# Optimization experiments

Measured on AMD Instinct MI355X. Metric: run time of the kernel, lower is better.

The kernel has to match this reference:

```python
import jax, jax.numpy as jnp
import numpy as np

N = 512      # state dim n
K = 8        # num_regimes
H = 256      # hidden dim for g0/g1/gate MLPs
B = 8192     # batch
INIT_SCALE = 0.1


def _mlp(x, w1, b1, w2, b2, w3, b3):
    # 2 hidden SiLU layers + linear head (matches ScalarMLP/GateNet with num_layers=2)
    h = jax.nn.silu(x @ w1 + b1)
    h = jax.nn.silu(h @ w2 + b2)
    return h @ w3 + b3


def setup_inputs() -> dict:
    key = jax.random.key(0)
    ks = jax.random.split(key, 12)

    def lin(k, fi, fo):
        kw, kb = jax.random.split(k)
        s = 1.0 / np.sqrt(fi)  # torch nn.Linear default init range
        w = jax.random.uniform(kw, (fi, fo), minval=-s, maxval=s, dtype=jnp.float32)
        b = jax.random.uniform(kb, (fo,), minval=-s, maxval=s, dtype=jnp.float32)
        return w, b

    g0_w1, g0_b1 = lin(ks[0], N, H)
    g0_w2, g0_b2 = lin(ks[1], H, H)
    g0_w3, g0_b3 = lin(ks[2], H, 1)
    g1_w1, g1_b1 = lin(ks[3], N, H)
    g1_w2, g1_b2 = lin(ks[4], H, H)
    g1_w3, g1_b3 = lin(ks[5], H, 1)
    gt_w1, gt_b1 = lin(ks[6], N, H)
    gt_w2, gt_b2 = lin(ks[7], H, H)
    gt_w3, gt_b3 = lin(ks[8], H, K)
    W = jax.random.uniform(ks[9], (K, N, N), minval=-INIT_SCALE, maxval=INIT_SCALE, dtype=jnp.float32)
    z = jax.random.normal(ks[10], (B, 2 * N), dtype=jnp.float32)
    return dict(z=z,
                g0_w1=g0_w1, g0_b1=g0_b1, g0_w2=g0_w2, g0_b2=g0_b2, g0_w3=g0_w3, g0_b3=g0_b3,
                g1_w1=g1_w1, g1_b1=g1_b1, g1_w2=g1_w2, g1_b2=g1_b2, g1_w3=g1_w3, g1_b3=g1_b3,
                gt_w1=gt_w1, gt_b1=gt_b1, gt_w2=gt_w2, gt_b2=gt_b2, gt_w3=gt_w3, gt_b3=gt_b3,
                W=W)


def reference(z,
              g0_w1, g0_b1, g0_w2, g0_b2, g0_w3, g0_b3,
              g1_w1, g1_b1, g1_w2, g1_b2, g1_w3, g1_b3,
              gt_w1, gt_b1, gt_w2, gt_b2, gt_w3, gt_b3,
              W):
    n = W.shape[-1]
    x0, x1 = z[:, :n], z[:, n:]

    def U(x0_, x1_):
        e0 = jnp.sum(_mlp(x0_, g0_w1, g0_b1, g0_w2, g0_b2, g0_w3, g0_b3))  # scalar
        e1 = jnp.sum(_mlp(x1_, g1_w1, g1_b1, g1_w2, g1_b2, g1_w3, g1_b3))
        alpha = jax.nn.softmax(_mlp(x0_, gt_w1, gt_b1, gt_w2, gt_b2, gt_w3, gt_b3), axis=-1)  # [B,K]
        # per-sample per-regime bilinear x1^T W_k x0 -> avoids materializing [B,n,n] W_eff
        q = jnp.einsum('bi,kij,bj->bk', x1_, W, x0_)
        return e0 + e1 + jnp.sum(alpha * q)

    grad_x0, grad_x1 = jax.grad(U, argnums=(0, 1))(x0, x1)
    return jnp.concatenate([-grad_x0, -grad_x1], axis=-1)  # [B, 2n]
```

## Files before the change

kernel.cpp:

```cpp
#include <hip/hip_runtime.h>
#include <cstdint>
#include <cstddef>

constexpr int BTOT = 8192, N = 512, H = 256, K = 8;

typedef __attribute__((ext_vector_type(8))) short short8v;
typedef __attribute__((ext_vector_type(4))) float f32x4;

__device__ __forceinline__ float bf2f(unsigned short u) {
    return __uint_as_float(((uint32_t)u) << 16);
}
__device__ __forceinline__ unsigned short f2bf(float f) {
    uint32_t u = __float_as_uint(f);
    uint32_t r = (u + 0x7FFFu + ((u >> 16) & 1u)) >> 16;
    return (unsigned short)r;
}

typedef __attribute__((address_space(3))) unsigned int lds_uint;
typedef __attribute__((address_space(1))) const unsigned int glob_uint;
__device__ __forceinline__ void async16(const unsigned short* g, unsigned short* l) {
    __builtin_amdgcn_global_load_lds((glob_uint*)g, (lds_uint*)l, 16, 0, 0);
}

struct GArg {
    const unsigned short* A;
    const unsigned short* Bt;
    const float* bias;
    const unsigned short* dmul;
    const float* alpha;
    const unsigned short* vsub;
    unsigned short* ob;
    unsigned short* ob2;
    float* of;
    int lda, ldbt, Ka, lddm, ldob, ldof;
};

enum { EPI_BF = 0, EPI_FWD = 1, EPI_BWD2 = 2, EPI_NEG = 3, EPI_NEGV = 4 };

template<int EPI>
__global__ __launch_bounds__(256) void gemm_g(GArg ga0, GArg ga1, GArg ga2)
{
    const int z = blockIdx.z;
    const GArg g = (z == 0) ? ga0 : (z == 1) ? ga1 : ga2;

    __shared__ __attribute__((aligned(16))) unsigned short As[3][128 * 32];
    __shared__ __attribute__((aligned(16))) unsigned short Bs[3][128 * 32];
    const int tid = threadIdx.x;
    const int lane = tid & 63, wave = tid >> 6;
    const int m0 = blockIdx.y * 128, n0 = blockIdx.x * 128;
    const int wr = (wave >> 1) * 64, wc = (wave & 1) * 64;
    const int rr = lane & 15;
    const int kb = ((lane >> 4) ^ (lane & 3)) << 3;

    const int r0 = tid >> 2;
    const int ko0 = (((tid & 3) ^ (r0 & 3)) << 3);
    const unsigned short* gA0 = g.A + (size_t)(m0 + r0) * g.lda + ko0;
    const unsigned short* gA1 = g.A + (size_t)(m0 + r0 + 64) * g.lda + ko0;
    const unsigned short* gB0 = g.Bt + (size_t)(n0 + r0) * g.ldbt + ko0;
    const unsigned short* gB1 = g.Bt + (size_t)(n0 + r0 + 64) * g.ldbt + ko0;

    auto stage = [&](int t, int buf) {
        const int k0 = t << 5;
        async16(gA0 + k0, &As[buf][tid * 8]);
        async16(gA1 + k0, &As[buf][(tid + 256) * 8]);
        async16(gB0 + k0, &Bs[buf][tid * 8]);
        async16(gB1 + k0, &Bs[buf][(tid + 256) * 8]);
    };

    f32x4 acc[4][4];
    #pragma unroll
    for (int i = 0; i < 4; ++i)
        #pragma unroll
        for (int j = 0; j < 4; ++j) acc[i][j] = (f32x4){0.f, 0.f, 0.f, 0.f};

    const int nt = g.Ka >> 5;

    stage(0, 0);
    if (nt > 1) stage(1, 1);

    int buf = 0;
    for (int t = 0; t < nt; ++t) {
        if (t + 1 < nt) { asm volatile("s_waitcnt vmcnt(4)" ::: "memory"); }
        else            { asm volatile("s_waitcnt vmcnt(0)" ::: "memory"); }
        __builtin_amdgcn_s_barrier();
        if (t + 2 < nt) {
            int b2 = buf + 2; if (b2 >= 3) b2 -= 3;
            stage(t + 2, b2);
        }
        short8v af[4], bfr[4];
        #pragma unroll
        for (int i = 0; i < 4; ++i)
            af[i] = *(const short8v*)(&As[buf][(wr + i * 16 + rr) * 32 + kb]);
        #pragma unroll
        for (int j = 0; j < 4; ++j)
            bfr[j] = *(const short8v*)(&Bs[buf][(wc + j * 16 + rr) * 32 + kb]);
        #pragma unroll
        for (int i = 0; i < 4; ++i)
            #pragma unroll
            for (int j = 0; j < 4; ++j)
                acc[i][j] = __builtin_amdgcn_mfma_f32_16x16x32_bf16(af[i], bfr[j], acc[i][j], 0, 0, 0);
        if (++buf == 3) buf = 0;
    }

    const int orow = (lane >> 4) * 4;
    #pragma unroll
    for (int i = 0; i < 4; ++i) {
        #pragma unroll
        for (int e = 0; e < 4; ++e) {
            const int row = m0 + wr + i * 16 + orow + e;
            if constexpr (EPI == EPI_NEGV) {
                float al[K];
                #pragma unroll
                for (int kk = 0; kk < K; ++kk) al[kk] = g.alpha[(size_t)row * K + kk];
                #pragma unroll
                for (int j = 0; j < 4; ++j) {
                    const int col = n0 + wc + rr + j * 16;
                    const unsigned short* vp = g.vsub + (size_t)row * (K * N) + col;
                    float sub = 0.f;
                    #pragma unroll
                    for (int kk = 0; kk < K; ++kk) sub += al[kk] * bf2f(vp[(size_t)kk * N]);
                    g.of[(size_t)row * g.ldof + col] = -acc[i][j][e] - sub;
                }
            } else {
                #pragma unroll
                for (int j = 0; j < 4; ++j) {
                    const int col = n0 + wc + rr + j * 16;
                    float v = acc[i][j][e];
                    if constexpr (EPI == EPI_BF) {
                        g.ob[(size_t)row * g.ldob + col] = f2bf(v);
                    } else if constexpr (EPI == EPI_FWD) {
                        float p = v + g.bias[col];
                        float s = 1.f / (1.f + expf(-p));
                        if (g.ob) g.ob[(size_t)row * g.ldob + col] = f2bf(p * s);
                        g.ob2[(size_t)row * g.ldob + col] = f2bf(s * (1.f + p * (1.f - s)));
                    } else if constexpr (EPI == EPI_BWD2) {
                        float t = v * bf2f(g.dmul[(size_t)row * g.lddm + col]);
                        g.ob[(size_t)row * g.ldob + col] = f2bf(t);
                    } else if constexpr (EPI == EPI_NEG) {
                        g.of[(size_t)row * g.ldof + col] -= v;
                    }
                }
            }
        }
    }
}

__global__ __launch_bounds__(256) void k_cvt_z(const float* __restrict__ z,
                                               unsigned short* __restrict__ o) {
    int g = (blockIdx.x * 256 + threadIdx.x) * 4;
    float4 v = *(const float4*)(z + g);
    ushort4 u;
    u.x = f2bf(v.x); u.y = f2bf(v.y); u.z = f2bf(v.z); u.w = f2bf(v.w);
    *(ushort4*)(o + g) = u;
}

__global__ __launch_bounds__(256) void k_transpose_w(const float* __restrict__ W,
    unsigned short* __restrict__ Wbf, unsigned short* __restrict__ WTbf)
{
    __shared__ float t[32][33];
    int k = blockIdx.z;
    int i0 = blockIdx.y * 32, j0 = blockIdx.x * 32;
    int tj = threadIdx.x & 31, ti = threadIdx.x >> 5;
    const float* Wk = W + (size_t)k * N * N;
    #pragma unroll
    for (int r = 0; r < 32; r += 8) {
        float v = Wk[(size_t)(i0 + ti + r) * N + j0 + tj];
        t[ti + r][tj] = v;
        Wbf[(size_t)k * N * N + (size_t)(i0 + ti + r) * N + j0 + tj] = f2bf(v);
    }
    __syncthreads();
    #pragma unroll
    for (int r = 0; r < 32; r += 8)
        WTbf[(size_t)k * N * N + (size_t)(j0 + ti + r) * N + i0 + tj] = f2bf(t[tj][ti + r]);
}

struct CvtJob { const float* src; unsigned short* dst; int ls, ld, cols32, tiles, trans; };
struct CvtTable { CvtJob j[12]; };

__global__ __launch_bounds__(256) void k_cvt_w(CvtTable T)
{
    int t = blockIdx.x;
    int ji = 0;
    while (t >= T.j[ji].tiles) { t -= T.j[ji].tiles; ++ji; }
    CvtJob jb = T.j[ji];
    int i0 = (t / jb.cols32) * 32, c0 = (t % jb.cols32) * 32;
    int tc = threadIdx.x & 31, tr = threadIdx.x >> 5;
    if (!jb.trans) {
        #pragma unroll
        for (int r = 0; r < 32; r += 8)
            jb.dst[(size_t)(i0 + tr + r) * jb.ld + c0 + tc] =
                f2bf(jb.src[(size_t)(i0 + tr + r) * jb.ls + c0 + tc]);
    } else {
        __shared__ float tt[32][33];
        #pragma unroll
        for (int r = 0; r < 32; r += 8)
            tt[tr + r][tc] = jb.src[(size_t)(i0 + tr + r) * jb.ls + c0 + tc];
        __syncthreads();
        #pragma unroll
        for (int r = 0; r < 32; r += 8)
            jb.dst[(size_t)(c0 + tr + r) * jb.ld + i0 + tc] = f2bf(tt[tc][tr + r]);
    }
}

__global__ __launch_bounds__(256) void k_head_s(const unsigned short* __restrict__ h2t,
    const float* __restrict__ w3t, const float* __restrict__ b3t,
    float* __restrict__ s)
{
    int t = threadIdx.x;
    int bl = t >> 3, k = t & 7;
    int b = blockIdx.x * 32 + bl;
    const unsigned short* ar = h2t + (size_t)b * H;
    float acc = b3t[k];
    for (int h0 = 0; h0 < H; h0 += 8) {
        short8v hv = *(const short8v*)(ar + h0);
        #pragma unroll
        for (int u = 0; u < 8; ++u)
            acc += bf2f((unsigned short)hv[u]) * w3t[(h0 + u) * K + k];
    }
    s[b * K + k] = acc;
}

__global__ __launch_bounds__(256) void k_q(const unsigned short* __restrict__ v0,
    const unsigned short* __restrict__ zb, float* __restrict__ q)
{
    int w = threadIdx.x >> 6, lane = threadIdx.x & 63;
    int idx = blockIdx.x * 4 + w;
    int b = idx >> 3, k = idx & 7;
    const unsigned short* vr = v0 + ((size_t)b * K + k) * N;
    const unsigned short* xr = zb + (size_t)b * 1024 + 512;
    short8v vv = *(const short8v*)(vr + lane * 8);
    short8v xv = *(const short8v*)(xr + lane * 8);
    float s = 0.f;
    #pragma unroll
    for (int t = 0; t < 8; ++t)
        s += bf2f((unsigned short)vv[t]) * bf2f((unsigned short)xv[t]);
    for (int off = 32; off; off >>= 1) s += __shfl_down(s, off, 64);
    if (lane == 0) q[idx] = s;
}

__global__ __launch_bounds__(256) void k_d(const float* __restrict__ s,
    const float* __restrict__ q, float* __restrict__ alpha,
    float* __restrict__ dd, int Bc)
{
    int b = blockIdx.x * 256 + threadIdx.x;
    if (b >= Bc) return;
    float sv[K], qv[K];
    float m = -1e30f;
    #pragma unroll
    for (int k = 0; k < K; ++k) { sv[k] = s[b * K + k]; m = fmaxf(m, sv[k]); }
    float sum = 0.f;
    #pragma unroll
    for (int k = 0; k < K; ++k) { sv[k] = expf(sv[k] - m); sum += sv[k]; }
    float inv = 1.f / sum, qbar = 0.f;
    #pragma unroll
    for (int k = 0; k < K; ++k) { sv[k] *= inv; qv[k] = q[b * K + k]; qbar += sv[k] * qv[k]; }
    #pragma unroll
    for (int k = 0; k < K; ++k) {
        alpha[b * K + k] = sv[k];
        dd[b * K + k] = sv[k] * (qv[k] - qbar);
    }
}

__global__ __launch_bounds__(256) void k_u2(
    const unsigned short* __restrict__ d2_0, const unsigned short* __restrict__ d2_1,
    const unsigned short* __restrict__ d2_t,
    const float* __restrict__ w3_0, const float* __restrict__ w3_1,
    const float* __restrict__ w3t, const float* __restrict__ dd,
    unsigned short* __restrict__ u2_0, unsigned short* __restrict__ u2_1,
    unsigned short* __restrict__ u2_t)
{
    int g = blockIdx.x * 256 + threadIdx.x;
    int h = g & (H - 1), b = g >> 8;
    u2_0[g] = f2bf(w3_0[h] * bf2f(d2_0[g]));
    u2_1[g] = f2bf(w3_1[h] * bf2f(d2_1[g]));
    float s = 0.f;
    #pragma unroll
    for (int k = 0; k < K; ++k) s += w3t[h * K + k] * dd[b * K + k];
    u2_t[g] = f2bf(s * bf2f(d2_t[g]));
}

__global__ __launch_bounds__(256) void k_gxq2(const unsigned short* __restrict__ v0,
    const unsigned short* __restrict__ v1, const float* __restrict__ alpha,
    float* __restrict__ out)
{
    int g = blockIdx.x * 256 + threadIdx.x;
    int b = g >> 6, jb = (g & 63) << 3;
    float al[K];
    #pragma unroll
    for (int k = 0; k < K; ++k) al[k] = alpha[b * K + k];
    const unsigned short* pv0 = v0 + (size_t)b * K * N + jb;
    const unsigned short* pv1 = v1 + (size_t)b * K * N + jb;
    float s0[8] = {}, s1[8] = {};
    #pragma unroll
    for (int k = 0; k < K; ++k) {
        short8v w1 = *(const short8v*)(pv1 + (size_t)k * N);
        short8v w0 = *(const short8v*)(pv0 + (size_t)k * N);
        #pragma unroll
        for (int t = 0; t < 8; ++t) {
            s0[t] += al[k] * bf2f((unsigned short)w1[t]);
            s1[t] += al[k] * bf2f((unsigned short)w0[t]);
        }
    }
    float* o0 = out + (size_t)b * 1024 + jb;
    float* o1 = o0 + 512;
    float4 x0 = *(float4*)o0, x1 = *(float4*)(o0 + 4);
    x0.x -= s0[0]; x0.y -= s0[1]; x0.z -= s0[2]; x0.w -= s0[3];
    x1.x -= s0[4]; x1.y -= s0[5]; x1.z -= s0[6]; x1.w -= s0[7];
    *(float4*)o0 = x0; *(float4*)(o0 + 4) = x1;
    float4 y0 = *(float4*)o1, y1 = *(float4*)(o1 + 4);
    y0.x -= s1[0]; y0.y -= s1[1]; y0.z -= s1[2]; y0.w -= s1[3];
    y1.x -= s1[4]; y1.y -= s1[5]; y1.z -= s1[6]; y1.w -= s1[7];
    *(float4*)o1 = y0; *(float4*)(o1 + 4) = y1;
}

extern "C" void kernel_launch(void* const* d_in, const int* in_sizes, int n_in,
                              void* d_out, int out_size, void* d_ws, size_t ws_size,
                              hipStream_t stream) {
    const float* z     = (const float*)d_in[0];
    const float* g0_w1 = (const float*)d_in[1];  const float* g0_b1 = (const float*)d_in[2];
    const float* g0_w2 = (const float*)d_in[3];  const float* g0_b2 = (const float*)d_in[4];
    const float* g0_w3 = (const float*)d_in[5];
    const float* g1_w1 = (const float*)d_in[7];  const float* g1_b1 = (const float*)d_in[8];
    const float* g1_w2 = (const float*)d_in[9];  const float* g1_b2 = (const float*)d_in[10];
    const float* g1_w3 = (const float*)d_in[11];
    const float* gt_w1 = (const float*)d_in[13]; const float* gt_b1 = (const float*)d_in[14];
    const float* gt_w2 = (const float*)d_in[15]; const float* gt_b2 = (const float*)d_in[16];
    const float* gt_w3 = (const float*)d_in[17]; const float* gt_b3 = (const float*)d_in[18];
    const float* W     = (const float*)d_in[19];
    float* out = (float*)d_out;

    char* wsb = (char*)d_ws;
    size_t off = 0;
    auto aus = [&](size_t n) -> unsigned short* {
        unsigned short* r = (unsigned short*)(wsb + off);
        off += ((n * 2 + 255) & ~(size_t)255);
        return r;
    };
    auto af4 = [&](size_t n) -> float* {
        float* r = (float*)(wsb + off);
        off += ((n * 4 + 255) & ~(size_t)255);
        return r;
    };

    unsigned short* Zbf  = aus((size_t)BTOT * 1024);
    unsigned short* Wbf  = aus((size_t)K * N * N);
    unsigned short* WTbf = aus((size_t)K * N * N);
    unsigned short* w1T[3], *w2T[3], *w2N[3];
    for (int i = 0; i < 3; ++i) w1T[i] = aus((size_t)H * N);
    for (int i = 0; i < 3; ++i) w2T[i] = aus((size_t)H * H);
    for (int i = 0; i < 3; ++i) w2N[i] = aus((size_t)H * H);
    unsigned short* w1N1  = aus((size_t)N * H);
    unsigned short* w1cat = aus((size_t)N * 2 * H);
    unsigned short* h1[3], *d1b[3], *d2b[3], *u2[3];
    for (int i = 0; i < 3; ++i) h1[i]  = aus((size_t)BTOT * H);
    for (int i = 0; i < 3; ++i) d1b[i] = aus((size_t)BTOT * H);
    for (int i = 0; i < 3; ++i) d2b[i] = aus((size_t)BTOT * H);
    for (int i = 0; i < 3; ++i) u2[i]  = aus((size_t)BTOT * H);
    unsigned short* h2t   = aus((size_t)BTOT * H);
    unsigned short* t2cat = aus((size_t)BTOT * 512);
    unsigned short* t21   = aus((size_t)BTOT * H);
    float* sbuf = af4((size_t)BTOT * K);
    float* qbuf = af4((size_t)BTOT * K);
    float* abuf = af4((size_t)BTOT * K);
    float* dbuf = af4((size_t)BTOT * K);

    int Bcv = BTOT;
    while (off + 2 * (((size_t)Bcv * K * N * 2 + 255) & ~(size_t)255) > ws_size && Bcv > 128)
        Bcv >>= 1;
    unsigned short* v0 = aus((size_t)Bcv * K * N);
    unsigned short* v1 = aus((size_t)Bcv * K * N);
    const bool full = (Bcv == BTOT);

    const dim3 blk(256);

    if (!full)
        hipMemsetAsync(d_out, 0, (size_t)out_size * sizeof(float), stream);

    k_cvt_z<<<BTOT * 1024 / (256 * 4), blk, 0, stream>>>(z, Zbf);
    k_transpose_w<<<dim3(N / 32, N / 32, K), blk, 0, stream>>>(W, Wbf, WTbf);

    CvtTable T;
    int nj = 0, tot = 0;
    auto addjob = [&](const float* src, int ls, unsigned short* dst, int ld,
                      int rows, int cols, int trans) {
        CvtJob jb; jb.src = src; jb.dst = dst; jb.ls = ls; jb.ld = ld;
        jb.cols32 = cols / 32; jb.tiles = (rows / 32) * (cols / 32); jb.trans = trans;
        T.j[nj++] = jb; tot += jb.tiles;
    };
    addjob(g0_w1, H, w1T[0], N, N, H, 1);
    addjob(g1_w1, H, w1T[1], N, N, H, 1);
    addjob(gt_w1, H, w1T[2], N, N, H, 1);
    addjob(g0_w2, H, w2T[0], H, H, H, 1);
    addjob(g1_w2, H, w2T[1], H, H, H, 1);
    addjob(gt_w2, H, w2T[2], H, H, H, 1);
    addjob(g0_w2, H, w2N[0], H, H, H, 0);
    addjob(g1_w2, H, w2N[1], H, H, H, 0);
    addjob(gt_w2, H, w2N[2], H, H, H, 0);
    addjob(g1_w1, H, w1N1, H, N, H, 0);
    addjob(g0_w1, H, w1cat, 2 * H, N, H, 0);
    addjob(gt_w1, H, w1cat + H, 2 * H, N, H, 0);
    k_cvt_w<<<tot, blk, 0, stream>>>(T);

    auto mk = [](const unsigned short* A, int lda, const unsigned short* Bt, int ldbt, int Ka) {
        GArg g; g.A = A; g.Bt = Bt; g.bias = nullptr; g.dmul = nullptr;
        g.alpha = nullptr; g.vsub = nullptr;
        g.ob = nullptr; g.ob2 = nullptr; g.of = nullptr;
        g.lda = lda; g.ldbt = ldbt; g.Ka = Ka; g.lddm = 0; g.ldob = 0; g.ldof = 0;
        return g;
    };

    {
        const float* bs[3] = {g0_b1, g1_b1, gt_b1};
        GArg a[3];
        for (int i = 0; i < 3; ++i) {
            a[i] = mk(Zbf + (i == 1 ? 512 : 0), 1024, w1T[i], N, N);
            a[i].bias = bs[i]; a[i].ob = h1[i]; a[i].ob2 = d1b[i]; a[i].ldob = H;
        }
        gemm_g<EPI_FWD><<<dim3(H / 128, BTOT / 128, 3), blk, 0, stream>>>(a[0], a[1], a[2]);
    }
    {
        const float* bs[3] = {g0_b2, g1_b2, gt_b2};
        GArg a[3];
        for (int i = 0; i < 3; ++i) {
            a[i] = mk(h1[i], H, w2T[i], H, H);
            a[i].bias = bs[i]; a[i].ob = (i == 2) ? h2t : nullptr;
            a[i].ob2 = d2b[i]; a[i].ldob = H;
        }
        gemm_g<EPI_FWD><<<dim3(H / 128, BTOT / 128, 3), blk, 0, stream>>>(a[0], a[1], a[2]);
    }
    k_head_s<<<BTOT / 32, blk, 0, stream>>>(h2t, gt_w3, gt_b3, sbuf);

    for (int cb = 0; cb < BTOT; cb += Bcv) {
        GArg a[2];
        a[0] = mk(Zbf + (size_t)cb * 1024, 1024, Wbf, N, N);
        a[0].ob = v0; a[0].ldob = K * N;
        a[1] = mk(Zbf + (size_t)cb * 1024 + 512, 1024, WTbf, N, N);
        a[1].ob = v1; a[1].ldob = K * N;
        gemm_g<EPI_BF><<<dim3(K * N / 128, Bcv / 128, 2), blk, 0, stream>>>(a[0], a[1], a[1]);

        k_q<<<Bcv * K / 4, blk, 0, stream>>>(v0, Zbf + (size_t)cb * 1024, qbuf + (size_t)cb * K);
        k_d<<<(Bcv + 255) / 256, blk, 0, stream>>>(sbuf + (size_t)cb * K, qbuf + (size_t)cb * K,
                                                   abuf + (size_t)cb * K, dbuf + (size_t)cb * K, Bcv);
        if (!full)
            k_gxq2<<<Bcv * 64 / 256, blk, 0, stream>>>(v0, v1, abuf + (size_t)cb * K,
                                                       out + (size_t)cb * 1024);
    }

    k_u2<<<BTOT * H / 256, blk, 0, stream>>>(d2b[0], d2b[1], d2b[2],
                                             g0_w3, g1_w3, gt_w3, dbuf,
                                             u2[0], u2[1], u2[2]);

    {
        GArg a[3];
        a[0] = mk(u2[0], H, w2N[0], H, H);
        a[0].dmul = d1b[0]; a[0].lddm = H; a[0].ob = t2cat;     a[0].ldob = 512;
        a[1] = mk(u2[1], H, w2N[1], H, H);
        a[1].dmul = d1b[1]; a[1].lddm = H; a[1].ob = t21;       a[1].ldob = H;
        a[2] = mk(u2[2], H, w2N[2], H, H);
        a[2].dmul = d1b[2]; a[2].lddm = H; a[2].ob = t2cat + H; a[2].ldob = 512;
        gemm_g<EPI_BWD2><<<dim3(H / 128, BTOT / 128, 3), blk, 0, stream>>>(a[0], a[1], a[2]);
    }
    {
        GArg a[2];
        a[0] = mk(t2cat, 512, w1cat, 2 * H, 512);
        a[0].of = out;       a[0].ldof = 1024;
        a[1] = mk(t21, H, w1N1, H, H);
        a[1].of = out + 512; a[1].ldof = 1024;
        if (full) {
            a[0].alpha = abuf; a[0].vsub = v1;
            a[1].alpha = abuf; a[1].vsub = v0;
            gemm_g<EPI_NEGV><<<dim3(N / 128, BTOT / 128, 2), blk, 0, stream>>>(a[0], a[1], a[1]);
        } else {
            gemm_g<EPI_NEG><<<dim3(N / 128, BTOT / 128, 2), blk, 0, stream>>>(a[0], a[1], a[1]);
        }
    }
}
```

Measured before the change: 246.1 us.

## Fuse bilinear V-GEMM with layer-1 MLP GEMMs and split final epilogue

In the full-batch path, the bilinear V projection GEMMs (z against W and W^T) and the three first-layer MLP GEMMs now run in one combined launch, indexed by block x. This removes a launch and lets the small MLP tiles fill the device alongside the large bilinear tiles. The final gradient GEMM no longer does the alpha-weighted V subtraction in its epilogue. It writes -acc, and a separate k_gxq2 kernel subtracts the bilinear term afterwards. That adds a kernel and an extra pass over out, in exchange for a lighter GEMM epilogue.

```diff
diff --git a/kernel.cpp b/kernel.cpp
--- a/kernel.cpp
+++ b/kernel.cpp
@@ -27,27 +27,21 @@
     const unsigned short* Bt;
     const float* bias;
     const unsigned short* dmul;
-    const float* alpha;
-    const unsigned short* vsub;
     unsigned short* ob;
     unsigned short* ob2;
     float* of;
     int lda, ldbt, Ka, lddm, ldob, ldof;
 };
-
-enum { EPI_BF = 0, EPI_FWD = 1, EPI_BWD2 = 2, EPI_NEG = 3, EPI_NEGV = 4 };
+struct GPack { GArg g[5]; };
+
+enum { EPI_BF = 0, EPI_FWD = 1, EPI_BWD2 = 2, EPI_NEG = 3, EPI_NEGW = 4 };
 
 template<int EPI>
-__global__ __launch_bounds__(256) void gemm_g(GArg ga0, GArg ga1, GArg ga2)
-{
-    const int z = blockIdx.z;
-    const GArg g = (z == 0) ? ga0 : (z == 1) ? ga1 : ga2;
-
-    __shared__ __attribute__((aligned(16))) unsigned short As[3][128 * 32];
-    __shared__ __attribute__((aligned(16))) unsigned short Bs[3][128 * 32];
+__device__ __forceinline__ void gemm_body(const GArg& g, int m0, int n0,
+                                          unsigned short* As, unsigned short* Bs)
+{
     const int tid = threadIdx.x;
     const int lane = tid & 63, wave = tid >> 6;
-    const int m0 = blockIdx.y * 128, n0 = blockIdx.x * 128;
     const int wr = (wave >> 1) * 64, wc = (wave & 1) * 64;
     const int rr = lane & 15;
     const int kb = ((lane >> 4) ^ (lane & 3)) << 3;
@@ -61,10 +55,10 @@
 
     auto stage = [&](int t, int buf) {
         const int k0 = t << 5;
-        async16(gA0 + k0, &As[buf][tid * 8]);
-        async16(gA1 + k0, &As[buf][(tid + 256) * 8]);
-        async16(gB0 + k0, &Bs[buf][tid * 8]);
-        async16(gB1 + k0, &Bs[buf][(tid + 256) * 8]);
+        async16(gA0 + k0, As + buf * 4096 + tid * 8);
+        async16(gA1 + k0, As + buf * 4096 + (tid + 256) * 8);
+        async16(gB0 + k0, Bs + buf * 4096 + tid * 8);
+        async16(gB1 + k0, Bs + buf * 4096 + (tid + 256) * 8);
     };
 
     f32x4 acc[4][4];
@@ -90,10 +84,10 @@
         short8v af[4], bfr[4];
         #pragma unroll
         for (int i = 0; i < 4; ++i)
-            af[i] = *(const short8v*)(&As[buf][(wr + i * 16 + rr) * 32 + kb]);
+            af[i] = *(const short8v*)(As + buf * 4096 + (wr + i * 16 + rr) * 32 + kb);
         #pragma unroll
         for (int j = 0; j < 4; ++j)
-            bfr[j] = *(const short8v*)(&Bs[buf][(wc + j * 16 + rr) * 32 + kb]);
+            bfr[j] = *(const short8v*)(Bs + buf * 4096 + (wc + j * 16 + rr) * 32 + kb);
         #pragma unroll
         for (int i = 0; i < 4; ++i)
             #pragma unroll
@@ -108,40 +102,49 @@
         #pragma unroll
         for (int e = 0; e < 4; ++e) {
             const int row = m0 + wr + i * 16 + orow + e;
-            if constexpr (EPI == EPI_NEGV) {
-                float al[K];
-                #pragma unroll
-                for (int kk = 0; kk < K; ++kk) al[kk] = g.alpha[(size_t)row * K + kk];
-                #pragma unroll
-                for (int j = 0; j < 4; ++j) {
-                    const int col = n0 + wc + rr + j * 16;
-                    const unsigned short* vp = g.vsub + (size_t)row * (K * N) + col;
-                    float sub = 0.f;
-                    #pragma unroll
-                    for (int kk = 0; kk < K; ++kk) sub += al[kk] * bf2f(vp[(size_t)kk * N]);
-                    g.of[(size_t)row * g.ldof + col] = -acc[i][j][e] - sub;
-                }
-            } else {
-                #pragma unroll
-                for (int j = 0; j < 4; ++j) {
-                    const int col = n0 + wc + rr + j * 16;
-                    float v = acc[i][j][e];
-                    if constexpr (EPI == EPI_BF) {
-                        g.ob[(size_t)row * g.ldob + col] = f2bf(v);
-                    } else if constexpr (EPI == EPI_FWD) {
-                        float p = v + g.bias[col];
-                        float s = 1.f / (1.f + expf(-p));
-                        if (g.ob) g.ob[(size_t)row * g.ldob + col] = f2bf(p * s);
-                        g.ob2[(size_t)row * g.ldob + col] = f2bf(s * (1.f + p * (1.f - s)));
-                    } else if constexpr (EPI == EPI_BWD2) {
-                        float t = v * bf2f(g.dmul[(size_t)row * g.lddm + col]);
-                        g.ob[(size_t)row * g.ldob + col] = f2bf(t);
-                    } else if constexpr (EPI == EPI_NEG) {
-                        g.of[(size_t)row * g.ldof + col] -= v;
-                    }
+            #pragma unroll
+            for (int j = 0; j < 4; ++j) {
+                const int col = n0 + wc + rr + j * 16;
+                float v = acc[i][j][e];
+                if constexpr (EPI == EPI_BF) {
+                    g.ob[(size_t)row * g.ldob + col] = f2bf(v);
+                } else if constexpr (EPI == EPI_FWD) {
+                    float p = v + g.bias[col];
+                    float s = 1.f / (1.f + expf(-p));
+                    if (g.ob) g.ob[(size_t)row * g.ldob + col] = f2bf(p * s);
+                    g.ob2[(size_t)row * g.ldob + col] = f2bf(s * (1.f + p * (1.f - s)));
+                } else if constexpr (EPI == EPI_BWD2) {
+                    float t = v * bf2f(g.dmul[(size_t)row * g.lddm + col]);
+                    g.ob[(size_t)row * g.ldob + col] = f2bf(t);
+                } else if constexpr (EPI == EPI_NEG) {
+                    g.of[(size_t)row * g.ldof + col] -= v;
+                } else {
+                    g.of[(size_t)row * g.ldof + col] = -v;
                 }
             }
         }
+    }
+}
+
+template<int EPI>
+__global__ __launch_bounds__(256) void gemm_g(GArg ga0, GArg ga1, GArg ga2)
+{
+    __shared__ __attribute__((aligned(16))) unsigned short As[3 * 128 * 32];
+    __shared__ __attribute__((aligned(16))) unsigned short Bs[3 * 128 * 32];
+    const int z = blockIdx.z;
+    const GArg g = (z == 0) ? ga0 : (z == 1) ? ga1 : ga2;
+    gemm_body<EPI>(g, blockIdx.y * 128, blockIdx.x * 128, As, Bs);
+}
+
+__global__ __launch_bounds__(256) void gemm_l1bil(GPack P)
+{
+    __shared__ __attribute__((aligned(16))) unsigned short As[3 * 128 * 32];
+    __shared__ __attribute__((aligned(16))) unsigned short Bs[3 * 128 * 32];
+    const int xb = blockIdx.x;
+    if (xb < 32) {
+        gemm_body<EPI_BF>(P.g[blockIdx.z], blockIdx.y * 128, xb * 128, As, Bs);
+    } else {
+        gemm_body<EPI_FWD>(P.g[2 + (xb - 32)], blockIdx.y * 128, blockIdx.z * 128, As, Bs);
     }
 }
 
@@ -403,21 +406,34 @@
 
     auto mk = [](const unsigned short* A, int lda, const unsigned short* Bt, int ldbt, int Ka) {
         GArg g; g.A = A; g.Bt = Bt; g.bias = nullptr; g.dmul = nullptr;
-        g.alpha = nullptr; g.vsub = nullptr;
         g.ob = nullptr; g.ob2 = nullptr; g.of = nullptr;
         g.lda = lda; g.ldbt = ldbt; g.Ka = Ka; g.lddm = 0; g.ldob = 0; g.ldof = 0;
         return g;
     };
 
-    {
-        const float* bs[3] = {g0_b1, g1_b1, gt_b1};
+    const float* bs1[3] = {g0_b1, g1_b1, gt_b1};
+
+    if (full) {
+        GPack P;
+        P.g[0] = mk(Zbf, 1024, Wbf, N, N);
+        P.g[0].ob = v0; P.g[0].ldob = K * N;
+        P.g[1] = mk(Zbf + 512, 1024, WTbf, N, N);
+        P.g[1].ob = v1; P.g[1].ldob = K * N;
+        for (int i = 0; i < 3; ++i) {
+            P.g[2 + i] = mk(Zbf + (i == 1 ? 512 : 0), 1024, w1T[i], N, N);
+            P.g[2 + i].bias = bs1[i]; P.g[2 + i].ob = h1[i];
+            P.g[2 + i].ob2 = d1b[i];  P.g[2 + i].ldob = H;
+        }
+        gemm_l1bil<<<dim3(35, BTOT / 128, 2), blk, 0, stream>>>(P);
+    } else {
         GArg a[3];
         for (int i = 0; i < 3; ++i) {
             a[i] = mk(Zbf + (i == 1 ? 512 : 0), 1024, w1T[i], N, N);
-            a[i].bias = bs[i]; a[i].ob = h1[i]; a[i].ob2 = d1b[i]; a[i].ldob = H;
+            a[i].bias = bs1[i]; a[i].ob = h1[i]; a[i].ob2 = d1b[i]; a[i].ldob = H;
         }
         gemm_g<EPI_FWD><<<dim3(H / 128, BTOT / 128, 3), blk, 0, stream>>>(a[0], a[1], a[2]);
     }
+
     {
         const float* bs[3] = {g0_b2, g1_b2, gt_b2};
         GArg a[3];
@@ -431,13 +447,14 @@
     k_head_s<<<BTOT / 32, blk, 0, stream>>>(h2t, gt_w3, gt_b3, sbuf);
 
     for (int cb = 0; cb < BTOT; cb += Bcv) {
-        GArg a[2];
-        a[0] = mk(Zbf + (size_t)cb * 1024, 1024, Wbf, N, N);
-        a[0].ob = v0; a[0].ldob = K * N;
-        a[1] = mk(Zbf + (size_t)cb * 1024 + 512, 1024, WTbf, N, N);
-        a[1].ob = v1; a[1].ldob = K * N;
-        gemm_g<EPI_BF><<<dim3(K * N / 128, Bcv / 128, 2), blk, 0, stream>>>(a[0], a[1], a[1]);
-
+        if (!full) {
+            GArg a[2];
+            a[0] = mk(Zbf + (size_t)cb * 1024, 1024, Wbf, N, N);
+            a[0].ob = v0; a[0].ldob = K * N;
+            a[1] = mk(Zbf + (size_t)cb * 1024 + 512, 1024, WTbf, N, N);
+            a[1].ob = v1; a[1].ldob = K * N;
+            gemm_g<EPI_BF><<<dim3(K * N / 128, Bcv / 128, 2), blk, 0, stream>>>(a[0], a[1], a[1]);
+        }
         k_q<<<Bcv * K / 4, blk, 0, stream>>>(v0, Zbf + (size_t)cb * 1024, qbuf + (size_t)cb * K);
         k_d<<<(Bcv + 255) / 256, blk, 0, stream>>>(sbuf + (size_t)cb * K, qbuf + (size_t)cb * K,
                                                    abuf + (size_t)cb * K, dbuf + (size_t)cb * K, Bcv);
@@ -467,9 +484,8 @@
         a[1] = mk(t21, H, w1N1, H, H);
         a[1].of = out + 512; a[1].ldof = 1024;
         if (full) {
-            a[0].alpha = abuf; a[0].vsub = v1;
-            a[1].alpha = abuf; a[1].vsub = v0;
-            gemm_g<EPI_NEGV><<<dim3(N / 128, BTOT / 128, 2), blk, 0, stream>>>(a[0], a[1], a[1]);
+            gemm_g<EPI_NEGW><<<dim3(N / 128, BTOT / 128, 2), blk, 0, stream>>>(a[0], a[1], a[1]);
+            k_gxq2<<<BTOT * 64 / 256, blk, 0, stream>>>(v0, v1, abuf, out);
         } else {
             gemm_g<EPI_NEG><<<dim3(N / 128, BTOT / 128, 2), blk, 0, stream>>>(a[0], a[1], a[1]);
         }
```

Result: slower. 265.3 us (+7.8%).
